# Kernel optimization log

Hardware: AMD Instinct MI355X
Metric: run time of the kernel (lower is better)

The kernel has to match this reference:

```python
import jax, jax.numpy as jnp
import numpy as np

HEADS = 4
DIM_HEAD = 32


def setup_inputs() -> dict:
    key = jax.random.key(0)
    k1, k2, k3, k4 = jax.random.split(key, 4)
    b, c, H, W, D = 2, 64, 48, 48, 48
    hidden = HEADS * DIM_HEAD  # 128
    return {
        "x": jax.random.normal(k1, (b, c, H, W, D), dtype=jnp.float32),
        "W_qkv": jax.random.normal(k2, (3 * hidden, c), dtype=jnp.float32) * 0.05,
        "W_out": jax.random.normal(k3, (c, hidden), dtype=jnp.float32) * 0.05,
        "b_out": jax.random.normal(k4, (c,), dtype=jnp.float32) * 0.05,
    }


def reference(x, W_qkv, W_out, b_out):
    b, c, H, W, D = x.shape
    n = H * W * D  # flattened spatial positions
    scale = DIM_HEAD ** (-0.5)

    xf = x.reshape(b, c, n)
    # 1x1x1 conv (no bias) == channel matmul
    qkv = jnp.einsum('bcn,oc->bon', xf, W_qkv)  # [b, 3*hidden, n]
    q, k, v = jnp.split(qkv, 3, axis=1)

    def to_heads(t):
        return t.reshape(b, HEADS, DIM_HEAD, n)

    q = to_heads(q) * scale                       # [b,h,d,n]
    k = jax.nn.softmax(to_heads(k), axis=-1)      # softmax over positions
    v = to_heads(v)

    context = jnp.einsum('bhdn,bhen->bhde', k, v)  # [b,h,d,e] tiny per-head matrix
    out = jnp.einsum('bhde,bhdn->bhen', context, q)  # [b,h,e,n]
    out = out.reshape(b, HEADS * DIM_HEAD, n)

    # 1x1x1 output conv with bias
    y = jnp.einsum('bhn,oh->bon', out, W_out) + b_out[None, :, None]
    return y.reshape(b, c, H, W, D)
```

## Files before the change

kernel.cpp:

```cpp
#include <hip/hip_runtime.h>
#include <math.h>

#define CIN 64
#define NP 128

typedef float f32x4 __attribute__((ext_vector_type(4)));
typedef short s16x8 __attribute__((ext_vector_type(8)));
typedef short s16x4 __attribute__((ext_vector_type(4)));

union FragU { s16x8 v; unsigned u[4]; };
union Frag4 { s16x4 v; unsigned u[2]; };

static __device__ __forceinline__ unsigned short f2b(float f) {
    unsigned u = __builtin_bit_cast(unsigned, f);
    unsigned r = (u + 0x7FFFu + ((u >> 16) & 1u)) >> 16;
    return (unsigned short)r;
}
static __device__ __forceinline__ unsigned pack2(float lo, float hi) {
    return (unsigned)f2b(lo) | ((unsigned)f2b(hi) << 16);
}

static __device__ __forceinline__ f32x4 mfma16(s16x4 a, s16x4 b, f32x4 c) {
#if __has_builtin(__builtin_amdgcn_mfma_f32_16x16x16bf16_1k)
    return __builtin_amdgcn_mfma_f32_16x16x16bf16_1k(a, b, c, 0, 0, 0);
#else
    asm volatile("v_mfma_f32_16x16x16_bf16 %0, %1, %2, %0\n\ts_nop 7\n\ts_nop 7"
                 : "+v"(c) : "v"(a), "v"(b));
    return c;
#endif
}

__global__ __launch_bounds__(256) void prep_w(const float* __restrict__ Wqkv,
                                              unsigned short* __restrict__ Wb) {
    int e0 = (blockIdx.x * 256 + threadIdx.x) * 8;
    int lane = (e0 >> 3) & 63;
    int kc = (e0 >> 9) & 1;
    int t = e0 >> 10;
    int row = 128 + t * 16 + (lane & 15);
    int c0 = kc * 32 + (lane >> 4) * 8;
    for (int j = 0; j < 8; ++j)
        Wb[e0 + j] = f2b(Wqkv[row * 64 + c0 + j]);
}

__global__ __launch_bounds__(256, 3) void lin_attn_ctx(
    const float* __restrict__ x, const unsigned short* __restrict__ Wb,
    float* __restrict__ P, int n, int nch)
{
    __shared__ float RED[4224];

    const int tid = threadIdx.x;
    const int l = tid & 63;
    const int w = tid >> 6;
    const int h = blockIdx.x;
    const int b = blockIdx.y;
    const int slot = blockIdx.z;
    const int nslot = gridDim.z;
    const int l15 = l & 15, lg = l >> 4;
    const uint4* Wb4 = (const uint4*)Wb;

    f32x4 zero4 = {0.f, 0.f, 0.f, 0.f};
    f32x4 ctx[2][2];
    float sacc[2] = {0.f, 0.f};
#pragma unroll
    for (int a = 0; a < 2; ++a)
#pragma unroll
        for (int c2 = 0; c2 < 2; ++c2) ctx[a][c2] = zero4;

    s16x8 ak[2][2], av[2][2];
#pragma unroll
    for (int rt = 0; rt < 2; ++rt)
#pragma unroll
        for (int kc = 0; kc < 2; ++kc) {
            ak[rt][kc] = *(const s16x8*)&Wb4[((2 * h + rt) * 2 + kc) * 64 + l];
            av[rt][kc] = *(const s16x8*)&Wb4[((8 + 2 * h + rt) * 2 + kc) * 64 + l];
        }

    const float* xw = x + (size_t)b * CIN * n;

    for (int ch = slot; ch < nch; ch += nslot) {
        const float* xp = xw + ch * NP + w * 32 + l15;
        s16x8 bx[2][2];
#pragma unroll
        for (int pt = 0; pt < 2; ++pt)
#pragma unroll
            for (int kc = 0; kc < 2; ++kc) {
                float xv[8];
#pragma unroll
                for (int j = 0; j < 8; ++j)
                    xv[j] = xp[(size_t)(kc * 32 + lg * 8 + j) * n + pt * 16];
                FragU fu;
#pragma unroll
                for (int i = 0; i < 4; ++i)
                    fu.u[i] = pack2(xv[2 * i], xv[2 * i + 1]);
                bx[pt][kc] = fu.v;
            }

        Frag4 ekf[2][2], vf[2][2];
#pragma unroll
        for (int pt = 0; pt < 2; ++pt) {
#pragma unroll
            for (int rt = 0; rt < 2; ++rt) {
                f32x4 z = zero4;
                z = __builtin_amdgcn_mfma_f32_16x16x32_bf16(bx[pt][0], ak[rt][0], z, 0, 0, 0);
                z = __builtin_amdgcn_mfma_f32_16x16x32_bf16(bx[pt][1], ak[rt][1], z, 0, 0, 0);
                f32x4 z2 = zero4;
                z2 = __builtin_amdgcn_mfma_f32_16x16x32_bf16(bx[pt][0], av[rt][0], z2, 0, 0, 0);
                z2 = __builtin_amdgcn_mfma_f32_16x16x32_bf16(bx[pt][1], av[rt][1], z2, 0, 0, 0);
                float e0 = __expf(z[0]), e1 = __expf(z[1]);
                float e2 = __expf(z[2]), e3 = __expf(z[3]);
                sacc[rt] += (e0 + e1) + (e2 + e3);
                Frag4 fe; fe.u[0] = pack2(e0, e1); fe.u[1] = pack2(e2, e3);
                ekf[pt][rt] = fe;
                Frag4 fv; fv.u[0] = pack2(z2[0], z2[1]); fv.u[1] = pack2(z2[2], z2[3]);
                vf[pt][rt] = fv;
            }
        }
#pragma unroll
        for (int rt = 0; rt < 2; ++rt)
#pragma unroll
            for (int vt = 0; vt < 2; ++vt) {
                ctx[rt][vt] = mfma16(ekf[0][rt].v, vf[0][vt].v, ctx[rt][vt]);
                ctx[rt][vt] = mfma16(ekf[1][rt].v, vf[1][vt].v, ctx[rt][vt]);
            }
    }

    float* Xf = RED;
    float* Sf = RED + 4096;
    float* Pb = P + (size_t)(b * nslot + slot) * 4224;
#pragma unroll
    for (int rt = 0; rt < 2; ++rt)
#pragma unroll
        for (int vt = 0; vt < 2; ++vt)
#pragma unroll
            for (int r = 0; r < 4; ++r) {
                int d = rt * 16 + lg * 4 + r, e = vt * 16 + l15;
                Xf[w * 1024 + d * 32 + e] = ctx[rt][vt][r];
            }
#pragma unroll
    for (int rt = 0; rt < 2; ++rt) {
        float s = sacc[rt];
        s += __shfl_xor(s, 16);
        s += __shfl_xor(s, 32);
        if (l < 16) Sf[w * 32 + rt * 16 + l15] = s;
    }
    __syncthreads();
    for (int i = tid; i < 1024; i += 256)
        Pb[h * 1056 + i] = Xf[i] + Xf[1024 + i] + Xf[2048 + i] + Xf[3072 + i];
    if (tid < 32)
        Pb[h * 1056 + 1024 + tid] = Sf[tid] + Sf[32 + tid] + Sf[64 + tid] + Sf[96 + tid];
}

__global__ __launch_bounds__(256) void reduce_p1(
    const float* __restrict__ P, float* __restrict__ P2, int nblk)
{
    const int idx = blockIdx.x * 256 + threadIdx.x;
    if (idx >= 4224) return;
    const int b = blockIdx.z, sz = blockIdx.y;
    float acc = 0.f;
    for (int slot = sz; slot < nblk; slot += 16)
        acc += P[((size_t)(b * nblk + slot)) * 4224 + idx];
    P2[((size_t)(b * 16 + sz)) * 4224 + idx] = acc;
}

__global__ __launch_bounds__(256) void reduce_p2(
    const float* __restrict__ P2, float* __restrict__ R)
{
    const int idx = blockIdx.x * 256 + threadIdx.x;
    if (idx >= 4224) return;
    const int b = blockIdx.y;
    float acc = 0.f;
#pragma unroll
    for (int s = 0; s < 16; ++s)
        acc += P2[((size_t)(b * 16 + s)) * 4224 + idx];
    R[b * 4224 + idx] = acc;
}

__global__ __launch_bounds__(256) void build_M(
    const float* __restrict__ R, const float* __restrict__ Wout,
    const float* __restrict__ Wqkv, float* __restrict__ Mt)
{
    __shared__ float ctx[4096];
    __shared__ float Ash[8 * 128];
    const int b = blockIdx.y;
    const int o0 = blockIdx.x * 8;
    const int tid = threadIdx.x;
    const float* Rb = R + b * 4224;
    for (int i = tid; i < 4096; i += 256) {
        const int hh = i >> 10, rr = i & 1023, e = rr >> 5, d = rr & 31;
        ctx[i] = Rb[hh * 1056 + d * 32 + e] / Rb[hh * 1056 + 1024 + d];
    }
    __syncthreads();
    for (int i = tid; i < 1024; i += 256) {
        const int oo = i >> 7, m = i & 127, hh = m >> 5, d = m & 31;
        float acc = 0.f;
#pragma unroll
        for (int e = 0; e < 32; ++e)
            acc += Wout[(o0 + oo) * 128 + hh * 32 + e] * ctx[hh * 1024 + e * 32 + d];
        Ash[i] = acc;
    }
    __syncthreads();
    const float scale = 0.17677669529663687f;
    for (int i = tid; i < 512; i += 256) {
        const int oo = i >> 6, c = i & 63;
        float acc = 0.f;
#pragma unroll
        for (int m = 0; m < 128; ++m)
            acc += Ash[oo * 128 + m] * Wqkv[m * 64 + c];
        Mt[b * 4096 + c * 64 + (o0 + oo)] = acc * scale;
    }
}

__global__ __launch_bounds__(256, 4) void final_proj(
    const float* __restrict__ x, const float* __restrict__ Mt,
    const float* __restrict__ bout, float* __restrict__ y, int n)
{
    const int b = blockIdx.y;
    const int p = blockIdx.x * 256 + threadIdx.x;
    const float* xb = x + (size_t)b * CIN * n + p;
    const float* M = Mt + b * 4096;
    float acc[64];
#pragma unroll
    for (int o = 0; o < 64; ++o) acc[o] = bout[o];
    for (int c = 0; c < 64; ++c) {
        const float xv = xb[(size_t)c * n];
        const float* Mr = M + c * 64;
#pragma unroll
        for (int o = 0; o < 64; ++o) acc[o] += Mr[o] * xv;
    }
    float* yb = y + (size_t)b * CIN * n + p;
#pragma unroll
    for (int o = 0; o < 64; ++o) yb[(size_t)o * n] = acc[o];
}

extern "C" void kernel_launch(void* const* d_in, const int* in_sizes, int n_in,
                              void* d_out, int out_size, void* d_ws, size_t ws_size,
                              hipStream_t stream) {
    const float* x    = (const float*)d_in[0];
    const float* Wqkv = (const float*)d_in[1];
    const float* Wout = (const float*)d_in[2];
    const float* bout = (const float*)d_in[3];
    float* y = (float*)d_out;

    const int n = in_sizes[0] / 128;
    const int nch = n / NP;

    int BLKX = 432;
    for (;;) {
        size_t need = 32768 + (size_t)2 * BLKX * 4224 * 4
                    + (size_t)2 * 16 * 4224 * 4
                    + 2 * 4224 * 4 + 2 * 4096 * 4;
        if (need <= ws_size || BLKX <= 64) break;
        BLKX = (BLKX == 432) ? 256 : (BLKX >> 1);
    }
    unsigned short* Wb = (unsigned short*)d_ws;
    float* P  = (float*)((char*)d_ws + 32768);
    float* P2 = P + (size_t)2 * BLKX * 4224;
    float* R  = P2 + (size_t)2 * 16 * 4224;
    float* Mt = R + 2 * 4224;

    prep_w<<<8, 256, 0, stream>>>(Wqkv, Wb);
    lin_attn_ctx<<<dim3(4, 2, BLKX), 256, 0, stream>>>(x, Wb, P, n, nch);
    reduce_p1<<<dim3(17, 16, 2), 256, 0, stream>>>(P, P2, BLKX);
    reduce_p2<<<dim3(17, 2), 256, 0, stream>>>(P2, R);
    build_M<<<dim3(8, 2), 256, 0, stream>>>(R, Wout, Wqkv, Mt);
    final_proj<<<dim3(n / 256, 2), 256, 0, stream>>>(x, Mt, bout, y, n);
}
```

Measured before the change: 97.33 us.

## Map heads to warps so each x tile is read once for all heads

Work is split differently: each block now covers all four heads, one per wavefront, over a 32-position subchunk. Before, each block handled one head and the same x tile was reloaded by four separate head blocks. Each warp writes its partial context straight to global memory, which drops the LDS reduction and the block barrier. The second reduce kernel is folded into build_M, and the K and V weight fragments are now loaded inside the loop with a sched_barrier to lower register pressure so occupancy can reach 4. The cost is reloading weight fragments on every iteration and smaller units of work per slot.

```diff
diff --git a/kernel.cpp b/kernel.cpp
--- a/kernel.cpp
+++ b/kernel.cpp
@@ -2,7 +2,6 @@
 #include <math.h>
 
 #define CIN 64
-#define NP 128
 
 typedef float f32x4 __attribute__((ext_vector_type(4)));
 typedef short s16x8 __attribute__((ext_vector_type(8)));
@@ -42,19 +41,16 @@
         Wb[e0 + j] = f2b(Wqkv[row * 64 + c0 + j]);
 }
 
-__global__ __launch_bounds__(256, 3) void lin_attn_ctx(
+__global__ __launch_bounds__(256, 4) void lin_attn_ctx(
     const float* __restrict__ x, const unsigned short* __restrict__ Wb,
-    float* __restrict__ P, int n, int nch)
-{
-    __shared__ float RED[4224];
-
+    float* __restrict__ P, int n, int nsub)
+{
     const int tid = threadIdx.x;
     const int l = tid & 63;
-    const int w = tid >> 6;
-    const int h = blockIdx.x;
+    const int h = tid >> 6;
+    const int slot = blockIdx.x;
+    const int nslot = gridDim.x;
     const int b = blockIdx.y;
-    const int slot = blockIdx.z;
-    const int nslot = gridDim.z;
     const int l15 = l & 15, lg = l >> 4;
     const uint4* Wb4 = (const uint4*)Wb;
 
@@ -66,19 +62,10 @@
 #pragma unroll
         for (int c2 = 0; c2 < 2; ++c2) ctx[a][c2] = zero4;
 
-    s16x8 ak[2][2], av[2][2];
-#pragma unroll
-    for (int rt = 0; rt < 2; ++rt)
-#pragma unroll
-        for (int kc = 0; kc < 2; ++kc) {
-            ak[rt][kc] = *(const s16x8*)&Wb4[((2 * h + rt) * 2 + kc) * 64 + l];
-            av[rt][kc] = *(const s16x8*)&Wb4[((8 + 2 * h + rt) * 2 + kc) * 64 + l];
-        }
-
-    const float* xw = x + (size_t)b * CIN * n;
-
-    for (int ch = slot; ch < nch; ch += nslot) {
-        const float* xp = xw + ch * NP + w * 32 + l15;
+    const float* xw = x + (size_t)b * CIN * n + l15;
+
+    for (int sc = slot; sc < nsub; sc += nslot) {
+        const float* xp = xw + sc * 32;
         s16x8 bx[2][2];
 #pragma unroll
         for (int pt = 0; pt < 2; ++pt)
@@ -96,24 +83,45 @@
             }
 
         Frag4 ekf[2][2], vf[2][2];
-#pragma unroll
-        for (int pt = 0; pt < 2; ++pt) {
-#pragma unroll
-            for (int rt = 0; rt < 2; ++rt) {
-                f32x4 z = zero4;
-                z = __builtin_amdgcn_mfma_f32_16x16x32_bf16(bx[pt][0], ak[rt][0], z, 0, 0, 0);
-                z = __builtin_amdgcn_mfma_f32_16x16x32_bf16(bx[pt][1], ak[rt][1], z, 0, 0, 0);
-                f32x4 z2 = zero4;
-                z2 = __builtin_amdgcn_mfma_f32_16x16x32_bf16(bx[pt][0], av[rt][0], z2, 0, 0, 0);
-                z2 = __builtin_amdgcn_mfma_f32_16x16x32_bf16(bx[pt][1], av[rt][1], z2, 0, 0, 0);
-                float e0 = __expf(z[0]), e1 = __expf(z[1]);
-                float e2 = __expf(z[2]), e3 = __expf(z[3]);
-                sacc[rt] += (e0 + e1) + (e2 + e3);
-                Frag4 fe; fe.u[0] = pack2(e0, e1); fe.u[1] = pack2(e2, e3);
-                ekf[pt][rt] = fe;
-                Frag4 fv; fv.u[0] = pack2(z2[0], z2[1]); fv.u[1] = pack2(z2[2], z2[3]);
-                vf[pt][rt] = fv;
-            }
+        {
+            s16x8 ak[2][2];
+#pragma unroll
+            for (int rt = 0; rt < 2; ++rt)
+#pragma unroll
+                for (int kc = 0; kc < 2; ++kc)
+                    ak[rt][kc] = *(const s16x8*)&Wb4[((2 * h + rt) * 2 + kc) * 64 + l];
+#pragma unroll
+            for (int pt = 0; pt < 2; ++pt)
+#pragma unroll
+                for (int rt = 0; rt < 2; ++rt) {
+                    f32x4 z = zero4;
+                    z = __builtin_amdgcn_mfma_f32_16x16x32_bf16(bx[pt][0], ak[rt][0], z, 0, 0, 0);
+                    z = __builtin_amdgcn_mfma_f32_16x16x32_bf16(bx[pt][1], ak[rt][1], z, 0, 0, 0);
+                    float e0 = __expf(z[0]), e1 = __expf(z[1]);
+                    float e2 = __expf(z[2]), e3 = __expf(z[3]);
+                    sacc[rt] += (e0 + e1) + (e2 + e3);
+                    Frag4 fe; fe.u[0] = pack2(e0, e1); fe.u[1] = pack2(e2, e3);
+                    ekf[pt][rt] = fe;
+                }
+        }
+        __builtin_amdgcn_sched_barrier(0);
+        {
+            s16x8 av[2][2];
+#pragma unroll
+            for (int rt = 0; rt < 2; ++rt)
+#pragma unroll
+                for (int kc = 0; kc < 2; ++kc)
+                    av[rt][kc] = *(const s16x8*)&Wb4[((8 + 2 * h + rt) * 2 + kc) * 64 + l];
+#pragma unroll
+            for (int pt = 0; pt < 2; ++pt)
+#pragma unroll
+                for (int rt = 0; rt < 2; ++rt) {
+                    f32x4 z2 = zero4;
+                    z2 = __builtin_amdgcn_mfma_f32_16x16x32_bf16(bx[pt][0], av[rt][0], z2, 0, 0, 0);
+                    z2 = __builtin_amdgcn_mfma_f32_16x16x32_bf16(bx[pt][1], av[rt][1], z2, 0, 0, 0);
+                    Frag4 fv; fv.u[0] = pack2(z2[0], z2[1]); fv.u[1] = pack2(z2[2], z2[3]);
+                    vf[pt][rt] = fv;
+                }
         }
 #pragma unroll
         for (int rt = 0; rt < 2; ++rt)
@@ -124,9 +132,7 @@
             }
     }
 
-    float* Xf = RED;
-    float* Sf = RED + 4096;
-    float* Pb = P + (size_t)(b * nslot + slot) * 4224;
+    float* Pb = P + (size_t)(b * nslot + slot) * 4224 + h * 1056;
 #pragma unroll
     for (int rt = 0; rt < 2; ++rt)
 #pragma unroll
@@ -134,20 +140,15 @@
 #pragma unroll
             for (int r = 0; r < 4; ++r) {
                 int d = rt * 16 + lg * 4 + r, e = vt * 16 + l15;
-                Xf[w * 1024 + d * 32 + e] = ctx[rt][vt][r];
+                Pb[d * 32 + e] = ctx[rt][vt][r];
             }
 #pragma unroll
     for (int rt = 0; rt < 2; ++rt) {
         float s = sacc[rt];
         s += __shfl_xor(s, 16);
         s += __shfl_xor(s, 32);
-        if (l < 16) Sf[w * 32 + rt * 16 + l15] = s;
-    }
-    __syncthreads();
-    for (int i = tid; i < 1024; i += 256)
-        Pb[h * 1056 + i] = Xf[i] + Xf[1024 + i] + Xf[2048 + i] + Xf[3072 + i];
-    if (tid < 32)
-        Pb[h * 1056 + 1024 + tid] = Sf[tid] + Sf[32 + tid] + Sf[64 + tid] + Sf[96 + tid];
+        if (l < 16) Pb[1024 + rt * 16 + l15] = s;
+    }
 }
 
 __global__ __launch_bounds__(256) void reduce_p1(
@@ -162,32 +163,27 @@
     P2[((size_t)(b * 16 + sz)) * 4224 + idx] = acc;
 }
 
-__global__ __launch_bounds__(256) void reduce_p2(
-    const float* __restrict__ P2, float* __restrict__ R)
-{
-    const int idx = blockIdx.x * 256 + threadIdx.x;
-    if (idx >= 4224) return;
-    const int b = blockIdx.y;
-    float acc = 0.f;
-#pragma unroll
-    for (int s = 0; s < 16; ++s)
-        acc += P2[((size_t)(b * 16 + s)) * 4224 + idx];
-    R[b * 4224 + idx] = acc;
-}
-
 __global__ __launch_bounds__(256) void build_M(
-    const float* __restrict__ R, const float* __restrict__ Wout,
+    const float* __restrict__ P2, const float* __restrict__ Wout,
     const float* __restrict__ Wqkv, float* __restrict__ Mt)
 {
+    __shared__ float Rsh[4224];
     __shared__ float ctx[4096];
     __shared__ float Ash[8 * 128];
     const int b = blockIdx.y;
     const int o0 = blockIdx.x * 8;
     const int tid = threadIdx.x;
-    const float* Rb = R + b * 4224;
+    for (int i = tid; i < 4224; i += 256) {
+        float acc = 0.f;
+#pragma unroll
+        for (int s = 0; s < 16; ++s)
+            acc += P2[((size_t)(b * 16 + s)) * 4224 + i];
+        Rsh[i] = acc;
+    }
+    __syncthreads();
     for (int i = tid; i < 4096; i += 256) {
         const int hh = i >> 10, rr = i & 1023, e = rr >> 5, d = rr & 31;
-        ctx[i] = Rb[hh * 1056 + d * 32 + e] / Rb[hh * 1056 + 1024 + d];
+        ctx[i] = Rsh[hh * 1056 + d * 32 + e] / Rsh[hh * 1056 + 1024 + d];
     }
     __syncthreads();
     for (int i = tid; i < 1024; i += 256) {
@@ -242,26 +238,24 @@
     float* y = (float*)d_out;
 
     const int n = in_sizes[0] / 128;
-    const int nch = n / NP;
+    const int nsub = n / 32;
 
     int BLKX = 432;
     for (;;) {
         size_t need = 32768 + (size_t)2 * BLKX * 4224 * 4
                     + (size_t)2 * 16 * 4224 * 4
-                    + 2 * 4224 * 4 + 2 * 4096 * 4;
+                    + 2 * 4096 * 4;
         if (need <= ws_size || BLKX <= 64) break;
-        BLKX = (BLKX == 432) ? 256 : (BLKX >> 1);
+        BLKX >>= 1;
     }
     unsigned short* Wb = (unsigned short*)d_ws;
     float* P  = (float*)((char*)d_ws + 32768);
     float* P2 = P + (size_t)2 * BLKX * 4224;
-    float* R  = P2 + (size_t)2 * 16 * 4224;
-    float* Mt = R + 2 * 4224;
+    float* Mt = P2 + (size_t)2 * 16 * 4224;
 
     prep_w<<<8, 256, 0, stream>>>(Wqkv, Wb);
-    lin_attn_ctx<<<dim3(4, 2, BLKX), 256, 0, stream>>>(x, Wb, P, n, nch);
+    lin_attn_ctx<<<dim3(BLKX, 2), 256, 0, stream>>>(x, Wb, P, n, nsub);
     reduce_p1<<<dim3(17, 16, 2), 256, 0, stream>>>(P, P2, BLKX);
-    reduce_p2<<<dim3(17, 2), 256, 0, stream>>>(P2, R);
-    build_M<<<dim3(8, 2), 256, 0, stream>>>(R, Wout, Wqkv, Mt);
+    build_M<<<dim3(8, 2), 256, 0, stream>>>(P2, Wout, Wqkv, Mt);
     final_proj<<<dim3(n / 256, 2), 256, 0, stream>>>(x, Mt, bout, y, n);
 }
```

After: 95.03 us. 1.02x faster.
